# Performance work log

Hardware: AMD Instinct MI355X
Metric: run time of the kernel (lower is better)

The kernel has to match this reference:

```python
import jax, jax.numpy as jnp
import numpy as np

B, M, N = 2097152, 6, 3
SQUARINGS = 8   # fixed scaling: ||T||_F <~ sqrt(M) ~ 2.5, so ||A|| ~ 0.01 after scaling
ORDER = 12     # Taylor order; gives ~machine precision at this scaled norm


def _expm(T):
    """Batched matrix exponential via fixed scaling-and-squaring + Horner Taylor.
    T: [B, N, N]. Numerically matches torch.matrix_exp for these well-scaled inputs."""
    A = T / (2.0 ** SQUARINGS)
    I = jnp.eye(T.shape[-1], dtype=T.dtype)
    # Horner: exp(A) ~ I + A(I + A/2(I + ... (I + A/ORDER)))
    E = I + A / ORDER
    for k in range(ORDER - 1, 0, -1):
        E = I + jnp.matmul(A / k, E)
    for _ in range(SQUARINGS):
        E = jnp.matmul(E, E)
    return E


def setup_inputs() -> dict:
    key = jax.random.key(0)
    kx, kc, kp = jax.random.split(key, 3)
    x = jax.random.normal(kx, (B, N, 1), dtype=jnp.float32)
    c = jax.random.normal(kc, (B, M), dtype=jnp.float32)
    psi = jax.random.normal(kp, (M, N, N), dtype=jnp.float32) * 0.1
    # per-dictionary-element Frobenius normalization, as in __init__
    psi = psi / jnp.linalg.norm(psi.reshape(M, -1), axis=1)[:, None, None]
    return {"x": x, "c": c, "psi": psi}


def reference(x, c, psi):
    # T[b] = sum_m c[b,m] * psi[m]  -> [B, N, N]
    T = jnp.einsum('bm,mij->bij', c, psi)
    return jnp.matmul(_expm(T), x)  # [B, N, 1]
```

## Files before the change

kernel.cpp:

```cpp
#include <hip/hip_runtime.h>

__global__ __launch_bounds__(256) void expm_kernel(
    const float* __restrict__ x,
    const float* __restrict__ c,
    const float* __restrict__ psi,
    float* __restrict__ out)
{
    const int b = blockIdx.x * blockDim.x + threadIdx.x;

    const float2* c2 = reinterpret_cast<const float2*>(c + (size_t)b * 6);
    const float2 ca = c2[0], cb = c2[1], cc = c2[2];
    const float cm[6] = {ca.x, ca.y, cb.x, cb.y, cc.x, cc.y};

    float T[9];
#pragma unroll
    for (int j = 0; j < 9; ++j) {
        float s = cm[0] * psi[0 * 9 + j];
#pragma unroll
        for (int m = 1; m < 6; ++m) s = fmaf(cm[m], psi[m * 9 + j], s);
        T[j] = s;
    }

    const float trT = T[0] + T[4] + T[8];
    const float m01 = fmaf(T[0], T[4], -T[1] * T[3]);
    const float m02 = fmaf(T[0], T[8], -T[2] * T[6]);
    const float m12 = fmaf(T[4], T[8], -T[5] * T[7]);
    const float msT = m01 + m02 + m12;
    const float M10 = fmaf(T[3], T[8], -T[5] * T[6]);
    const float M20 = fmaf(T[3], T[7], -T[4] * T[6]);
    const float detT = fmaf(T[0], m12, fmaf(-T[1], M10, T[2] * M20));
    const float c2v = trT * 0.25f;
    const float c1v = msT * -0.0625f;
    const float c0v = detT * 0.015625f;

    const float d2 = fmaf(c2v, c2v, c1v);
    const float d1 = fmaf(c2v, c1v, c0v);
    const float d0 = c2v * c0v;

    const float tk[8] = {1.0f,
                         1.0f,
                         0.5f,
                         1.6666667e-1f,
                         4.1666667e-2f,
                         8.3333333e-3f,
                         1.3888889e-3f,
                         1.9841270e-4f};
    float b0 = 2.4801587e-5f, b1 = 0.0f, b2 = 0.0f;
#pragma unroll
    for (int k = 7; k >= 0; --k) {
        const float n0 = fmaf(b2, c0v, tk[k]);
        const float n1 = fmaf(b2, c1v, b0);
        const float n2 = fmaf(b2, c2v, b1);
        b0 = n0; b1 = n1; b2 = n2;
    }

#pragma unroll
    for (int s2 = 0; s2 < 2; ++s2) {
        const float q0 = b0 * b0;
        const float q1 = 2.0f * (b0 * b1);
        const float q2 = fmaf(b1, b1, 2.0f * (b0 * b2));
        const float q3 = 2.0f * (b1 * b2);
        const float q4 = b2 * b2;
        b0 = fmaf(d0, q4, fmaf(c0v, q3, q0));
        b1 = fmaf(d1, q4, fmaf(c1v, q3, q1));
        b2 = fmaf(d2, q4, fmaf(c2v, q3, q2));
    }
    const float b1q = b1 * 0.25f;
    const float b2q = b2 * 0.0625f;

    const float* xb = x + (size_t)b * 3;
    const float x0 = xb[0], x1 = xb[1], x2 = xb[2];
    const float w0 = fmaf(T[0], x0, fmaf(T[1], x1, T[2] * x2));
    const float w1 = fmaf(T[3], x0, fmaf(T[4], x1, T[5] * x2));
    const float w2 = fmaf(T[6], x0, fmaf(T[7], x1, T[8] * x2));
    const float v0 = fmaf(T[0], w0, fmaf(T[1], w1, T[2] * w2));
    const float v1 = fmaf(T[3], w0, fmaf(T[4], w1, T[5] * w2));
    const float v2 = fmaf(T[6], w0, fmaf(T[7], w1, T[8] * w2));

    float* ob = out + (size_t)b * 3;
    ob[0] = fmaf(b0, x0, fmaf(b1q, w0, b2q * v0));
    ob[1] = fmaf(b0, x1, fmaf(b1q, w1, b2q * v1));
    ob[2] = fmaf(b0, x2, fmaf(b1q, w2, b2q * v2));
}

extern "C" void kernel_launch(void* const* d_in, const int* in_sizes, int n_in,
                              void* d_out, int out_size, void* d_ws, size_t ws_size,
                              hipStream_t stream) {
    const float* x   = (const float*)d_in[0];
    const float* c   = (const float*)d_in[1];
    const float* psi = (const float*)d_in[2];
    float* out = (float*)d_out;

    const int B = in_sizes[1] / 6;
    const int block = 256;
    const int grid = B / block;
    expm_kernel<<<grid, block, 0, stream>>>(x, c, psi, out);
}
```

Baseline: 104.6 us.

## Vectorize loads, pack T accumulation into float2 FMAs, use nontemporal stores

```diff
diff --git a/kernel.cpp b/kernel.cpp
--- a/kernel.cpp
+++ b/kernel.cpp
@@ -1,4 +1,8 @@
 #include <hip/hip_runtime.h>
+
+typedef float v2f __attribute__((ext_vector_type(2)));
+typedef float v4u __attribute__((ext_vector_type(4), aligned(8)));
+typedef float v2u __attribute__((ext_vector_type(2), aligned(4)));
 
 __global__ __launch_bounds__(256) void expm_kernel(
     const float* __restrict__ x,
@@ -8,18 +12,37 @@
 {
     const int b = blockIdx.x * blockDim.x + threadIdx.x;
 
-    const float2* c2 = reinterpret_cast<const float2*>(c + (size_t)b * 6);
-    const float2 ca = c2[0], cb = c2[1], cc = c2[2];
-    const float cm[6] = {ca.x, ca.y, cb.x, cb.y, cc.x, cc.y};
+    const float* cb = c + (size_t)b * 6;
+    const v4u cv4 = *reinterpret_cast<const v4u*>(cb);
+    const v2u cv2 = *reinterpret_cast<const v2u*>(cb + 4);
+    const float cm[6] = {cv4.x, cv4.y, cv4.z, cv4.w, cv2.x, cv2.y};
 
-    float T[9];
+    const float* xb = x + (size_t)b * 3;
+    const v2u xv2 = *reinterpret_cast<const v2u*>(xb);
+    const float x0 = xv2.x, x1 = xv2.y, x2 = xb[2];
+
+    v2f T01, T23, T45, T67;
+    float T8;
+    {
+        const v2f cm0 = {cm[0], cm[0]};
+        T01 = cm0 * v2f{psi[0], psi[1]};
+        T23 = cm0 * v2f{psi[2], psi[3]};
+        T45 = cm0 * v2f{psi[4], psi[5]};
+        T67 = cm0 * v2f{psi[6], psi[7]};
+        T8  = cm[0] * psi[8];
 #pragma unroll
-    for (int j = 0; j < 9; ++j) {
-        float s = cm[0] * psi[0 * 9 + j];
-#pragma unroll
-        for (int m = 1; m < 6; ++m) s = fmaf(cm[m], psi[m * 9 + j], s);
-        T[j] = s;
+        for (int m = 1; m < 6; ++m) {
+            const v2f cmm = {cm[m], cm[m]};
+            const float* pm = psi + m * 9;
+            T01 = __builtin_elementwise_fma(cmm, v2f{pm[0], pm[1]}, T01);
+            T23 = __builtin_elementwise_fma(cmm, v2f{pm[2], pm[3]}, T23);
+            T45 = __builtin_elementwise_fma(cmm, v2f{pm[4], pm[5]}, T45);
+            T67 = __builtin_elementwise_fma(cmm, v2f{pm[6], pm[7]}, T67);
+            T8  = fmaf(cm[m], pm[8], T8);
+        }
     }
+    const float T[9] = {T01.x, T01.y, T23.x, T23.y, T45.x, T45.y,
+                        T67.x, T67.y, T8};
 
     const float trT = T[0] + T[4] + T[8];
     const float m01 = fmaf(T[0], T[4], -T[1] * T[3]);
@@ -37,14 +60,9 @@
     const float d1 = fmaf(c2v, c1v, c0v);
     const float d0 = c2v * c0v;
 
-    const float tk[8] = {1.0f,
-                         1.0f,
-                         0.5f,
-                         1.6666667e-1f,
-                         4.1666667e-2f,
-                         8.3333333e-3f,
-                         1.3888889e-3f,
-                         1.9841270e-4f};
+    const float tk[8] = {1.0f, 1.0f, 0.5f,
+                         1.6666667e-1f, 4.1666667e-2f, 8.3333333e-3f,
+                         1.3888889e-3f, 1.9841270e-4f};
     float b0 = 2.4801587e-5f, b1 = 0.0f, b2 = 0.0f;
 #pragma unroll
     for (int k = 7; k >= 0; --k) {
@@ -68,8 +86,6 @@
     const float b1q = b1 * 0.25f;
     const float b2q = b2 * 0.0625f;
 
-    const float* xb = x + (size_t)b * 3;
-    const float x0 = xb[0], x1 = xb[1], x2 = xb[2];
     const float w0 = fmaf(T[0], x0, fmaf(T[1], x1, T[2] * x2));
     const float w1 = fmaf(T[3], x0, fmaf(T[4], x1, T[5] * x2));
     const float w2 = fmaf(T[6], x0, fmaf(T[7], x1, T[8] * x2));
@@ -78,9 +94,9 @@
     const float v2 = fmaf(T[6], w0, fmaf(T[7], w1, T[8] * w2));
 
     float* ob = out + (size_t)b * 3;
-    ob[0] = fmaf(b0, x0, fmaf(b1q, w0, b2q * v0));
-    ob[1] = fmaf(b0, x1, fmaf(b1q, w1, b2q * v1));
-    ob[2] = fmaf(b0, x2, fmaf(b1q, w2, b2q * v2));
+    __builtin_nontemporal_store(fmaf(b0, x0, fmaf(b1q, w0, b2q * v0)), ob + 0);
+    __builtin_nontemporal_store(fmaf(b0, x1, fmaf(b1q, w1, b2q * v1)), ob + 1);
+    __builtin_nontemporal_store(fmaf(b0, x2, fmaf(b1q, w2, b2q * v2)), ob + 2);
 }
 
 extern "C" void kernel_launch(void* const* d_in, const int* in_sizes, int n_in,
```

Result: no change. 104.3 us (-0.3%).
